# Kernel optimization log

Hardware: AMD Instinct MI355X
Metric: run time of the kernel (lower is better)

## Reference

```python
import jax, jax.numpy as jnp
import numpy as np

SCALE = 100.0

def square_distance(src, dst):
    # src: [B,N,D], dst: [B,M,D] -> [B,N,M] squared euclidean distances
    d = -2.0 * jnp.einsum('bnd,bmd->bnm', src, dst)
    d = d + jnp.sum(src * src, axis=-1)[:, :, None]
    d = d + jnp.sum(dst * dst, axis=-1)[:, None, :]
    return d

def setup_inputs() -> dict:
    key = jax.random.key(0)
    k1, k2 = jax.random.split(key)
    B, N, M, D = 8, 8192, 8192, 3
    pred = jax.random.normal(k1, (B, N, D), dtype=jnp.float32)
    gt = jax.random.normal(k2, (B, M, D), dtype=jnp.float32)
    return {"pred": pred, "gt": gt}

def reference(pred, gt):
    dis = square_distance(pred, gt)              # [B,N,M]
    pred_to_gt = jnp.min(dis, axis=2).mean(axis=1)  # [B]
    gt_to_pred = jnp.min(dis, axis=1).mean(axis=1)  # [B]
    return (0.5 * pred_to_gt + 0.5 * gt_to_pred).mean() * SCALE
```

## Files before the change

kernel.cpp:

```cpp
#include <hip/hip_runtime.h>


#define B_DIM 8
#define N_DIM 8192
#define MT    (N_DIM / 32)
#define BLOCK 256
#define PPW   2

typedef short  bf16x8 __attribute__((ext_vector_type(8)));
typedef float  f32x16 __attribute__((ext_vector_type(16)));

__device__ __forceinline__ unsigned short bf16_rne(float f) {
    unsigned int u = __float_as_uint(f);
    u += 0x7fffu + ((u >> 16) & 1u);
    return (unsigned short)(u >> 16);
}
__device__ __forceinline__ float bf16f(unsigned short h) {
    return __uint_as_float(((unsigned int)h) << 16);
}

__global__ __launch_bounds__(256) void chamfer_prep(
    const float* __restrict__ pred, const float* __restrict__ gt,
    unsigned short* __restrict__ bpack, float* __restrict__ out)
{
    const int i   = blockIdx.x * 256 + threadIdx.x;
    if (i == 0) out[0] = 0.0f;
    const int dir = i >> 16;
    const int bm  = i & 0xFFFF;
    const float* dst = dir ? pred : gt;
    const float x = dst[3*bm+0], y = dst[3*bm+1], z = dst[3*bm+2];
    const unsigned short hx = bf16_rne(x), hy = bf16_rne(y), hz = bf16_rne(z);
    const unsigned short lx = bf16_rne(x - bf16f(hx));
    const unsigned short ly = bf16_rne(y - bf16f(hy));
    const unsigned short lz = bf16_rne(z - bf16f(hz));
    const float gn = x*x + y*y + z*z;
    const unsigned short gnh = bf16_rne(gn), gnl = bf16_rne(gn - bf16f(gnh));
    const unsigned short one = 0x3F80;

    const int b  = bm >> 13, m = bm & (N_DIM - 1);
    const int mt = m >> 5,   c = m & 31;
    const int dirb = (dir << 3) | b;
    unsigned short* p0 = bpack + ((size_t)(dirb * MT + mt) * 64 + c) * 8;
    unsigned short* p1 = p0 + 32 * 8;
    bf16x8 h0 = {(short)hx,(short)hy,(short)hz,(short)lx,(short)ly,(short)lz,(short)hx,(short)hy};
    bf16x8 h1 = {(short)hz,(short)one,(short)one,(short)gnh,(short)gnl,0,0,0};
    *(bf16x8*)p0 = h0;
    *(bf16x8*)p1 = h1;
}

__global__ __launch_bounds__(BLOCK, 4) void chamfer_partial(
    const float* __restrict__ pred, const float* __restrict__ gt,
    const bf16x8* __restrict__ bpack, float* __restrict__ out)
{
    __shared__ float cbuf[PPW * 16 * 128];
    __shared__ float wsum[2];
    const int dirb = blockIdx.x;
    const int dir  = dirb >> 3, b = dirb & 7;
    const int w    = threadIdx.x >> 6, lane = threadIdx.x & 63;
    const int halfk = lane >> 5,  col = lane & 31;
    const int nsub = w & 1;
    const int mh   = w >> 1;

    const float* src  = dir ? gt : pred;
    const float* srcb = src + (size_t)b * N_DIM * 3;

    bf16x8 afrag[PPW];
    #pragma unroll
    for (int p = 0; p < PPW; ++p) {
        const int ntile = blockIdx.y * 4 + nsub * 2 + p;
        const int n = ntile * 32 + col;
        const float x = srcb[3*n+0], y = srcb[3*n+1], z = srcb[3*n+2];
        const float ax = -2.f*x, ay = -2.f*y, az = -2.f*z;
        const unsigned short ahx = bf16_rne(ax), ahy = bf16_rne(ay), ahz = bf16_rne(az);
        const unsigned short alx = bf16_rne(ax - bf16f(ahx));
        const unsigned short aly = bf16_rne(ay - bf16f(ahy));
        const unsigned short alz = bf16_rne(az - bf16f(ahz));
        const float pn = x*x + y*y + z*z;
        const unsigned short pnh = bf16_rne(pn), pnl = bf16_rne(pn - bf16f(pnh));
        const unsigned short one = 0x3F80;
        bf16x8 a0 = {(short)ahx,(short)ahy,(short)ahz,(short)ahx,(short)ahy,(short)ahz,(short)alx,(short)aly};
        bf16x8 a1 = {(short)alz,(short)pnh,(short)pnl,(short)one,(short)one,0,0,0};
        afrag[p] = (halfk == 0) ? a0 : a1;
    }

    float best[PPW][16];
    #pragma unroll
    for (int p = 0; p < PPW; ++p)
        #pragma unroll
        for (int r = 0; r < 16; ++r) best[p][r] = 1e30f;

    const bf16x8* bw = bpack + (size_t)dirb * (MT * 64) + (size_t)(mh * 128) * 64 + lane;

    for (int t = 0; t < 64; ++t) {
        const bf16x8 c0 = bw[0];
        const bf16x8 c1 = bw[64];
        bw += 128;
        f32x16 d0, d1;
        asm volatile(
            "v_mfma_f32_32x32x16_bf16 %0, %2, %3, 0\n\t"
            "v_mfma_f32_32x32x16_bf16 %1, %2, %4, 0\n\t"
            "s_nop 7\n\t"
            "s_nop 3"
            : "=&v"(d0), "=&v"(d1)
            : "v"(afrag[0]), "v"(c0), "v"(c1));
        __builtin_amdgcn_sched_barrier(0x34);
        #pragma unroll
        for (int r = 0; r < 16; ++r)
            best[0][r] = fminf(fminf(best[0][r], d0[r]), d1[r]);
        f32x16 d2, d3;
        asm volatile(
            "v_mfma_f32_32x32x16_bf16 %0, %2, %3, 0\n\t"
            "v_mfma_f32_32x32x16_bf16 %1, %2, %4, 0\n\t"
            "s_nop 7\n\t"
            "s_nop 3"
            : "=&v"(d2), "=&v"(d3)
            : "v"(afrag[1]), "v"(c0), "v"(c1));
        __builtin_amdgcn_sched_barrier(0x34);
        #pragma unroll
        for (int r = 0; r < 16; ++r)
            best[1][r] = fminf(fminf(best[1][r], d2[r]), d3[r]);
    }

    if (mh == 1) {
        #pragma unroll
        for (int p = 0; p < PPW; ++p)
            #pragma unroll
            for (int r = 0; r < 16; ++r)
                cbuf[(p * 16 + r) * 128 + nsub * 64 + lane] = best[p][r];
    }
    __syncthreads();
    if (mh == 0) {
        float bsum = 0.f;
        #pragma unroll
        for (int p = 0; p < PPW; ++p) {
            float s = 0.f;
            #pragma unroll
            for (int r = 0; r < 16; ++r) {
                float v = fminf(best[p][r], cbuf[(p * 16 + r) * 128 + nsub * 64 + lane]);
                v = fminf(v, __shfl_xor(v, 1,  64));
                v = fminf(v, __shfl_xor(v, 2,  64));
                v = fminf(v, __shfl_xor(v, 4,  64));
                v = fminf(v, __shfl_xor(v, 8,  64));
                v = fminf(v, __shfl_xor(v, 16, 64));
                s += v;
            }
            bsum += s + __shfl_xor(s, 32, 64);
        }
        if (lane == 0) wsum[nsub] = bsum;
    }
    __syncthreads();
    if (threadIdx.x == 0) {
        const float scale = 100.0f * 0.5f / ((float)B_DIM * (float)N_DIM);
        atomicAdd(out, (wsum[0] + wsum[1]) * scale);
    }
}

extern "C" void kernel_launch(void* const* d_in, const int* in_sizes, int n_in,
                              void* d_out, int out_size, void* d_ws, size_t ws_size,
                              hipStream_t stream) {
    const float* pred = (const float*)d_in[0];
    const float* gt   = (const float*)d_in[1];
    float* out = (float*)d_out;
    unsigned short* bpack = (unsigned short*)d_ws;

    chamfer_prep<<<(2 * B_DIM * N_DIM) / 256, 256, 0, stream>>>(pred, gt, bpack, out);

    dim3 grid(16, N_DIM / 128);
    chamfer_partial<<<grid, BLOCK, 0, stream>>>(pred, gt, (const bf16x8*)bpack, out);
}
```

Baseline: 102.4 us.

## Fuse prep and partial kernels via cooperative launch with grid sync

Merges the packing kernel into the main chamfer kernel using a cooperative launch: each thread packs one point, then a grid-wide sync precedes the MFMA min loop. This removes one kernel launch and the inter-kernel gap. The cost is a grid barrier, and the cooperative launch requires all 1024 blocks to be co-resident. If the cooperative launch fails, the code falls back to the original two-kernel path.

```diff
diff --git a/kernel.cpp b/kernel.cpp
--- a/kernel.cpp
+++ b/kernel.cpp
@@ -1,4 +1,7 @@
 #include <hip/hip_runtime.h>
+#include <hip/hip_cooperative_groups.h>
+
+namespace cg = cooperative_groups;
 
 
 #define B_DIM 8
@@ -19,12 +22,10 @@
     return __uint_as_float(((unsigned int)h) << 16);
 }
 
-__global__ __launch_bounds__(256) void chamfer_prep(
+__device__ __forceinline__ void pack_point(
     const float* __restrict__ pred, const float* __restrict__ gt,
-    unsigned short* __restrict__ bpack, float* __restrict__ out)
+    unsigned short* __restrict__ bpack, int i)
 {
-    const int i   = blockIdx.x * 256 + threadIdx.x;
-    if (i == 0) out[0] = 0.0f;
     const int dir = i >> 16;
     const int bm  = i & 0xFFFF;
     const float* dst = dir ? pred : gt;
@@ -48,12 +49,18 @@
     *(bf16x8*)p1 = h1;
 }
 
-__global__ __launch_bounds__(BLOCK, 4) void chamfer_partial(
+__global__ __launch_bounds__(BLOCK, 4) void chamfer_fused(
     const float* __restrict__ pred, const float* __restrict__ gt,
-    const bf16x8* __restrict__ bpack, float* __restrict__ out)
+    unsigned short* __restrict__ bpack, float* __restrict__ out)
 {
     __shared__ float cbuf[PPW * 16 * 128];
     __shared__ float wsum[2];
+
+    const int gid = (blockIdx.y * 16 + blockIdx.x) * BLOCK + threadIdx.x;
+    if (gid == 0) out[0] = 0.0f;
+    if (gid < 2 * B_DIM * N_DIM) pack_point(pred, gt, bpack, gid);
+    __threadfence();
+
     const int dirb = blockIdx.x;
     const int dir  = dirb >> 3, b = dirb & 7;
     const int w    = threadIdx.x >> 6, lane = threadIdx.x & 63;
@@ -89,7 +96,10 @@
         #pragma unroll
         for (int r = 0; r < 16; ++r) best[p][r] = 1e30f;
 
-    const bf16x8* bw = bpack + (size_t)dirb * (MT * 64) + (size_t)(mh * 128) * 64 + lane;
+    cg::this_grid().sync();
+
+    const bf16x8* bw = (const bf16x8*)bpack
+                     + (size_t)dirb * (MT * 64) + (size_t)(mh * 128) * 64 + lane;
 
     for (int t = 0; t < 64; ++t) {
         const bf16x8 c0 = bw[0];
@@ -155,6 +165,122 @@
     }
 }
 
+__global__ __launch_bounds__(256) void chamfer_prep(
+    const float* __restrict__ pred, const float* __restrict__ gt,
+    unsigned short* __restrict__ bpack, float* __restrict__ out)
+{
+    const int i = blockIdx.x * 256 + threadIdx.x;
+    if (i == 0) out[0] = 0.0f;
+    pack_point(pred, gt, bpack, i);
+}
+
+__global__ __launch_bounds__(BLOCK, 4) void chamfer_partial(
+    const float* __restrict__ pred, const float* __restrict__ gt,
+    const bf16x8* __restrict__ bpack, float* __restrict__ out)
+{
+    __shared__ float cbuf[PPW * 16 * 128];
+    __shared__ float wsum[2];
+    const int dirb = blockIdx.x;
+    const int dir  = dirb >> 3, b = dirb & 7;
+    const int w    = threadIdx.x >> 6, lane = threadIdx.x & 63;
+    const int halfk = lane >> 5,  col = lane & 31;
+    const int nsub = w & 1;
+    const int mh   = w >> 1;
+
+    const float* src  = dir ? gt : pred;
+    const float* srcb = src + (size_t)b * N_DIM * 3;
+
+    bf16x8 afrag[PPW];
+    #pragma unroll
+    for (int p = 0; p < PPW; ++p) {
+        const int ntile = blockIdx.y * 4 + nsub * 2 + p;
+        const int n = ntile * 32 + col;
+        const float x = srcb[3*n+0], y = srcb[3*n+1], z = srcb[3*n+2];
+        const float ax = -2.f*x, ay = -2.f*y, az = -2.f*z;
+        const unsigned short ahx = bf16_rne(ax), ahy = bf16_rne(ay), ahz = bf16_rne(az);
+        const unsigned short alx = bf16_rne(ax - bf16f(ahx));
+        const unsigned short aly = bf16_rne(ay - bf16f(ahy));
+        const unsigned short alz = bf16_rne(az - bf16f(ahz));
+        const float pn = x*x + y*y + z*z;
+        const unsigned short pnh = bf16_rne(pn), pnl = bf16_rne(pn - bf16f(pnh));
+        const unsigned short one = 0x3F80;
+        bf16x8 a0 = {(short)ahx,(short)ahy,(short)ahz,(short)ahx,(short)ahy,(short)ahz,(short)alx,(short)aly};
+        bf16x8 a1 = {(short)alz,(short)pnh,(short)pnl,(short)one,(short)one,0,0,0};
+        afrag[p] = (halfk == 0) ? a0 : a1;
+    }
+
+    float best[PPW][16];
+    #pragma unroll
+    for (int p = 0; p < PPW; ++p)
+        #pragma unroll
+        for (int r = 0; r < 16; ++r) best[p][r] = 1e30f;
+
+    const bf16x8* bw = bpack + (size_t)dirb * (MT * 64) + (size_t)(mh * 128) * 64 + lane;
+
+    for (int t = 0; t < 64; ++t) {
+        const bf16x8 c0 = bw[0];
+        const bf16x8 c1 = bw[64];
+        bw += 128;
+        f32x16 d0, d1;
+        asm volatile(
+            "v_mfma_f32_32x32x16_bf16 %0, %2, %3, 0\n\t"
+            "v_mfma_f32_32x32x16_bf16 %1, %2, %4, 0\n\t"
+            "s_nop 7\n\t"
+            "s_nop 3"
+            : "=&v"(d0), "=&v"(d1)
+            : "v"(afrag[0]), "v"(c0), "v"(c1));
+        __builtin_amdgcn_sched_barrier(0x34);
+        #pragma unroll
+        for (int r = 0; r < 16; ++r)
+            best[0][r] = fminf(fminf(best[0][r], d0[r]), d1[r]);
+        f32x16 d2, d3;
+        asm volatile(
+            "v_mfma_f32_32x32x16_bf16 %0, %2, %3, 0\n\t"
+            "v_mfma_f32_32x32x16_bf16 %1, %2, %4, 0\n\t"
+            "s_nop 7\n\t"
+            "s_nop 3"
+            : "=&v"(d2), "=&v"(d3)
+            : "v"(afrag[1]), "v"(c0), "v"(c1));
+        __builtin_amdgcn_sched_barrier(0x34);
+        #pragma unroll
+        for (int r = 0; r < 16; ++r)
+            best[1][r] = fminf(fminf(best[1][r], d2[r]), d3[r]);
+    }
+
+    if (mh == 1) {
+        #pragma unroll
+        for (int p = 0; p < PPW; ++p)
+            #pragma unroll
+            for (int r = 0; r < 16; ++r)
+                cbuf[(p * 16 + r) * 128 + nsub * 64 + lane] = best[p][r];
+    }
+    __syncthreads();
+    if (mh == 0) {
+        float bsum = 0.f;
+        #pragma unroll
+        for (int p = 0; p < PPW; ++p) {
+            float s = 0.f;
+            #pragma unroll
+            for (int r = 0; r < 16; ++r) {
+                float v = fminf(best[p][r], cbuf[(p * 16 + r) * 128 + nsub * 64 + lane]);
+                v = fminf(v, __shfl_xor(v, 1,  64));
+                v = fminf(v, __shfl_xor(v, 2,  64));
+                v = fminf(v, __shfl_xor(v, 4,  64));
+                v = fminf(v, __shfl_xor(v, 8,  64));
+                v = fminf(v, __shfl_xor(v, 16, 64));
+                s += v;
+            }
+            bsum += s + __shfl_xor(s, 32, 64);
+        }
+        if (lane == 0) wsum[nsub] = bsum;
+    }
+    __syncthreads();
+    if (threadIdx.x == 0) {
+        const float scale = 100.0f * 0.5f / ((float)B_DIM * (float)N_DIM);
+        atomicAdd(out, (wsum[0] + wsum[1]) * scale);
+    }
+}
+
 extern "C" void kernel_launch(void* const* d_in, const int* in_sizes, int n_in,
                               void* d_out, int out_size, void* d_ws, size_t ws_size,
                               hipStream_t stream) {
@@ -163,8 +289,13 @@
     float* out = (float*)d_out;
     unsigned short* bpack = (unsigned short*)d_ws;
 
-    chamfer_prep<<<(2 * B_DIM * N_DIM) / 256, 256, 0, stream>>>(pred, gt, bpack, out);
-
-    dim3 grid(16, N_DIM / 128);
-    chamfer_partial<<<grid, BLOCK, 0, stream>>>(pred, gt, (const bf16x8*)bpack, out);
-}
+    void* args[4] = {(void*)&pred, (void*)&gt, (void*)&bpack, (void*)&out};
+    hipError_t err = hipLaunchCooperativeKernel(
+        (const void*)chamfer_fused, dim3(16, N_DIM / 128), dim3(BLOCK),
+        args, 0, stream);
+    if (err != hipSuccess) {
+        chamfer_prep<<<(2 * B_DIM * N_DIM) / 256, 256, 0, stream>>>(pred, gt, bpack, out);
+        dim3 grid(16, N_DIM / 128);
+        chamfer_partial<<<grid, BLOCK, 0, stream>>>(pred, gt, (const bf16x8*)bpack, out);
+    }
+}
```

Result: slower. 238.5 us (+132.9%).
